# Kernel tuning notes

Hardware: AMD Instinct MI355X
Metric: run time of the kernel (lower is better)

## Reference

```python
import jax, jax.numpy as jnp
import numpy as np

B, T, D_IN, D_OUT = 64, 1024, 512, 512


def setup_inputs() -> dict:
    key = jax.random.key(0)
    k_x, k_w, k_wr = jax.random.split(key, 3)
    x = jax.random.normal(k_x, (B, T, D_IN), dtype=jnp.float32)
    # glorot_uniform for W
    limit = np.sqrt(6.0 / (D_IN + D_OUT)).astype(np.float32)
    W = jax.random.uniform(k_w, (D_IN, D_OUT), dtype=jnp.float32, minval=-limit, maxval=limit)
    # orthogonal for W_recurrent
    a = jax.random.normal(k_wr, (D_OUT, D_OUT), dtype=jnp.float32)
    q, r = jnp.linalg.qr(a)
    W_recurrent = q * jnp.sign(jnp.diag(r))[None, :]
    b = jnp.zeros((D_OUT,), dtype=jnp.float32)
    return {"x": x, "W": W, "W_recurrent": W_recurrent, "b": b}


def reference(x, W, W_recurrent, b):
    # x: [B, T, D_in]; sequential tanh RNN; return last hidden state [B, D_out]
    x_t = jnp.transpose(x, (1, 0, 2))  # [T, B, D_in]
    h0 = jnp.zeros((x.shape[0], W.shape[1]), dtype=x.dtype)

    def step(h, xt):
        h_new = jnp.tanh(xt @ W + h @ W_recurrent + b)
        return h_new, None

    h_last, _ = jax.lax.scan(step, h0, x_t)
    return h_last
```

## Files before the change

kernel.cpp:

```cpp
#include <hip/hip_runtime.h>
#include <math.h>

#define BATCH   64
#define TSTEPS  1024
#define DIN     512
#define DH      512
#define MDIM    (BATCH * TSTEPS)

#define VPAIRS  184
#define LPAIRS  72
#define LSTRIDE 76
#define LDS_WORDS (512 * LSTRIDE + 2 * 256)
#define LDS_BYTES (LDS_WORDS * 4)

typedef _Float16 h2_t __attribute__((ext_vector_type(2)));

__device__ inline unsigned short f2h_bits(float x) {
    _Float16 h = (_Float16)x;
    return __builtin_bit_cast(unsigned short, h);
}

__device__ inline unsigned int pack2h(float lo, float hi) {
    return (unsigned int)f2h_bits(lo) | ((unsigned int)f2h_bits(hi) << 16);
}

__device__ inline float dot2h(unsigned int ha, unsigned int wb, float acc) {
#if __has_builtin(__builtin_amdgcn_fdot2)
    return __builtin_amdgcn_fdot2(__builtin_bit_cast(h2_t, ha),
                                  __builtin_bit_cast(h2_t, wb), acc, false);
#else
    float hl = (float)__builtin_bit_cast(h2_t, ha).x;
    float hh = (float)__builtin_bit_cast(h2_t, ha).y;
    float wl = (float)__builtin_bit_cast(h2_t, wb).x;
    float wh = (float)__builtin_bit_cast(h2_t, wb).y;
    return fmaf(hh, wh, fmaf(hl, wl, acc));
#endif
}

__global__ __launch_bounds__(256) void gemm_xw(const float* __restrict__ X,
                                               const float* __restrict__ W,
                                               const float* __restrict__ bias,
                                               float* __restrict__ XW) {
    __shared__ float As[16][68];
    __shared__ float Bs[16][68];

    const int tid = threadIdx.x;
    const int bx  = blockIdx.x & 7;
    const int by  = blockIdx.x >> 3;
    const int m0  = by * 64;
    const int n0  = bx * 64;

    const int ty = tid >> 4;
    const int tx = tid & 15;

    const int arow = tid >> 2;
    const int akq  = (tid & 3) * 4;
    const int brow = tid >> 4;
    const int bcq  = (tid & 15) * 4;

    float acc[4][4] = {{0.f}};

    for (int k0 = 0; k0 < DIN; k0 += 16) {
        float4 av = *(const float4*)&X[(size_t)(m0 + arow) * DIN + k0 + akq];
        float4 bv = *(const float4*)&W[(size_t)(k0 + brow) * DH + n0 + bcq];
        __syncthreads();
        As[akq + 0][arow] = av.x;
        As[akq + 1][arow] = av.y;
        As[akq + 2][arow] = av.z;
        As[akq + 3][arow] = av.w;
        *(float4*)&Bs[brow][bcq] = bv;
        __syncthreads();

        #pragma unroll
        for (int k = 0; k < 16; ++k) {
            float4 a = *(const float4*)&As[k][ty * 4];
            float4 b = *(const float4*)&Bs[k][tx * 4];
            float ar[4] = {a.x, a.y, a.z, a.w};
            float br[4] = {b.x, b.y, b.z, b.w};
            #pragma unroll
            for (int i = 0; i < 4; ++i)
                #pragma unroll
                for (int j = 0; j < 4; ++j)
                    acc[i][j] = fmaf(ar[i], br[j], acc[i][j]);
        }
    }

    float4 bv = *(const float4*)&bias[n0 + tx * 4];
    const float br[4] = {bv.x, bv.y, bv.z, bv.w};
    #pragma unroll
    for (int i = 0; i < 4; ++i) {
        float4 o;
        o.x = acc[i][0] + br[0];
        o.y = acc[i][1] + br[1];
        o.z = acc[i][2] + br[2];
        o.w = acc[i][3] + br[3];
        *(float4*)&XW[(size_t)(m0 + ty * 4 + i) * DH + n0 + tx * 4] = o;
    }
}

__global__ __launch_bounds__(512, 2) void rnn_scan2(const float* __restrict__ XW,
                                                    const float* __restrict__ Wr,
                                                    float* __restrict__ Hout) {
    extern __shared__ unsigned int lds[];
    unsigned int* wrl  = lds;
    unsigned int* hbuf = lds + 512 * LSTRIDE;

    const int b = blockIdx.x;
    const int j = threadIdx.x;

    unsigned int wreg[VPAIRS];
    #pragma unroll
    for (int p = 0; p < VPAIRS; ++p) {
        float lo = Wr[(size_t)(2 * p)     * DH + j];
        float hi = Wr[(size_t)(2 * p + 1) * DH + j];
        wreg[p] = pack2h(lo, hi);
    }
    unsigned int* wl_my = wrl + (size_t)j * LSTRIDE;
    #pragma unroll
    for (int p = 0; p < LPAIRS; ++p) {
        int r0 = 2 * (VPAIRS + p);
        float lo = Wr[(size_t)r0       * DH + j];
        float hi = Wr[(size_t)(r0 + 1) * DH + j];
        wl_my[p] = pack2h(lo, hi);
    }
    hbuf[j] = 0u;
    __syncthreads();

    const float* xwb = XW + (size_t)b * TSTEPS * DH + j;
    float xwv  = xwb[0];
    float h_f  = 0.0f;
    int   cur  = 0;

    const unsigned int* wl = wrl + (size_t)j * LSTRIDE;

    for (int t = 0; t < TSTEPS; ++t) {
        const unsigned int* hp = hbuf + cur * 256;

        const int tn = (t + 1 < TSTEPS) ? (t + 1) : (TSTEPS - 1);
        float xwn = xwb[(size_t)tn * DH];

        float a0 = 0.f, a1 = 0.f, a2 = 0.f, a3 = 0.f;

        #pragma unroll
        for (int p = 0; p < VPAIRS; p += 4) {
            uint4 hv = *(const uint4*)(hp + p);
            a0 = dot2h(hv.x, wreg[p + 0], a0);
            a1 = dot2h(hv.y, wreg[p + 1], a1);
            a2 = dot2h(hv.z, wreg[p + 2], a2);
            a3 = dot2h(hv.w, wreg[p + 3], a3);
        }
        #pragma unroll
        for (int p = 0; p < LPAIRS; p += 4) {
            uint4 hv = *(const uint4*)(hp + VPAIRS + p);
            uint4 wv = *(const uint4*)(wl + p);
            a0 = dot2h(hv.x, wv.x, a0);
            a1 = dot2h(hv.y, wv.y, a1);
            a2 = dot2h(hv.z, wv.z, a2);
            a3 = dot2h(hv.w, wv.w, a3);
        }

        float z = ((a0 + a1) + (a2 + a3)) + xwv;
        h_f = tanhf(z);

        unsigned short* hbn = (unsigned short*)(hbuf + ((cur ^ 1) * 256));
        hbn[j] = f2h_bits(h_f);

        __syncthreads();
        cur ^= 1;
        xwv = xwn;
    }

    Hout[(size_t)b * DH + j] = h_f;
}

extern "C" void kernel_launch(void* const* d_in, const int* in_sizes, int n_in,
                              void* d_out, int out_size, void* d_ws, size_t ws_size,
                              hipStream_t stream) {
    const float* x  = (const float*)d_in[0];
    const float* W  = (const float*)d_in[1];
    const float* Wr = (const float*)d_in[2];
    const float* bv = (const float*)d_in[3];
    float* out = (float*)d_out;

    const size_t xw_bytes = (size_t)MDIM * DH * sizeof(float);
    if (ws_size < xw_bytes) return;
    float* xw = (float*)d_ws;

    static int lds_attr_done = 0;
    (void)lds_attr_done;
    hipFuncSetAttribute((const void*)rnn_scan2,
                        hipFuncAttributeMaxDynamicSharedMemorySize, LDS_BYTES);

    gemm_xw<<<dim3((MDIM / 64) * (DH / 64)), dim3(256), 0, stream>>>(x, W, bv, xw);

    rnn_scan2<<<dim3(BATCH), dim3(512), LDS_BYTES, stream>>>(xw, Wr, out);
}
```

Before: 2.280 ms.

## Use MFMA fp16 input GEMM and readlane-broadcast hidden state in RNN scan

Converts x to fp16 and transposes W to fp16, then computes the input projection with MFMA 16x16x32 f16 instructions instead of the scalar fp32 GEMM. The scalar kernel stays as a fallback when the workspace is too small. The recurrent scan now loads each wave's hidden-state slice once and broadcasts elements with readlane rather than issuing many LDS loads per step. It also replaces tanhf with an exp2/rcp approximation. This adds two conversion kernels, lowers the precision of the input projection, and changes the tanh accuracy.

Result: slower. 2.516 ms (+10.4%).

```diff
diff --git a/kernel.cpp b/kernel.cpp
--- a/kernel.cpp
+++ b/kernel.cpp
@@ -7,23 +7,23 @@
 #define DH      512
 #define MDIM    (BATCH * TSTEPS)
 
-#define VPAIRS  184
-#define LPAIRS  72
-#define LSTRIDE 76
-#define LDS_WORDS (512 * LSTRIDE + 2 * 256)
-#define LDS_BYTES (LDS_WORDS * 4)
-
-typedef _Float16 h2_t __attribute__((ext_vector_type(2)));
+#define WREGW   180
+#define WLDSW   76
+#define WSTRIDE 76
+#define K2_LDS_WORDS (512 * WSTRIDE + 2 * 256)
+#define K2_LDS_BYTES (K2_LDS_WORDS * 4)
+
+typedef _Float16 h2_t  __attribute__((ext_vector_type(2)));
+typedef _Float16 f16x8 __attribute__((ext_vector_type(8)));
+typedef float    f32x4 __attribute__((ext_vector_type(4)));
 
 __device__ inline unsigned short f2h_bits(float x) {
     _Float16 h = (_Float16)x;
     return __builtin_bit_cast(unsigned short, h);
 }
-
 __device__ inline unsigned int pack2h(float lo, float hi) {
     return (unsigned int)f2h_bits(lo) | ((unsigned int)f2h_bits(hi) << 16);
 }
-
 __device__ inline float dot2h(unsigned int ha, unsigned int wb, float acc) {
 #if __has_builtin(__builtin_amdgcn_fdot2)
     return __builtin_amdgcn_fdot2(__builtin_bit_cast(h2_t, ha),
@@ -36,6 +36,133 @@
     return fmaf(hh, wh, fmaf(hl, wl, acc));
 #endif
 }
+__device__ inline unsigned int rl(unsigned int v, int lane) {
+    return (unsigned int)__builtin_amdgcn_readlane((int)v, lane);
+}
+__device__ inline float ftanh(float x) {
+    float e = __builtin_amdgcn_exp2f(x * 2.88539008177792681472f);
+    return 1.0f - 2.0f * __builtin_amdgcn_rcpf(e + 1.0f);
+}
+
+__global__ __launch_bounds__(256) void convert_x(const float* __restrict__ x,
+                                                 _Float16* __restrict__ xh,
+                                                 int nvec) {
+    int i = blockIdx.x * blockDim.x + threadIdx.x;
+    int stride = gridDim.x * blockDim.x;
+    for (; i < nvec; i += stride) {
+        const float4* p = (const float4*)x + 2 * (size_t)i;
+        float4 a = p[0], b = p[1];
+        f16x8 o = { (_Float16)a.x, (_Float16)a.y, (_Float16)a.z, (_Float16)a.w,
+                    (_Float16)b.x, (_Float16)b.y, (_Float16)b.z, (_Float16)b.w };
+        ((f16x8*)xh)[i] = o;
+    }
+}
+
+__global__ __launch_bounds__(256) void transpose_w(const float* __restrict__ W,
+                                                   _Float16* __restrict__ Wt) {
+    __shared__ float tile[64][65];
+    const int t  = threadIdx.x;
+    const int c  = t & 63;
+    const int r0 = t >> 6;
+    const int bn = blockIdx.x & 7;
+    const int bk = blockIdx.x >> 3;
+    const int k0 = bk * 64, n0 = bn * 64;
+    #pragma unroll
+    for (int i = 0; i < 16; ++i)
+        tile[r0 + 4 * i][c] = W[(size_t)(k0 + r0 + 4 * i) * DH + n0 + c];
+    __syncthreads();
+    #pragma unroll
+    for (int i = 0; i < 16; ++i)
+        Wt[(size_t)(n0 + r0 + 4 * i) * DIN + k0 + c] = (_Float16)tile[c][r0 + 4 * i];
+}
+
+__global__ __launch_bounds__(256) void gemm_xw_mfma(const _Float16* __restrict__ Xh,
+                                                    const _Float16* __restrict__ Wt,
+                                                    const float* __restrict__ bias,
+                                                    float* __restrict__ XW) {
+    __shared__ __align__(16) _Float16 Ah[128][32];
+    __shared__ __align__(16) _Float16 Bh[128][32];
+
+    const int tid  = threadIdx.x;
+    const int wv   = tid >> 6;
+    const int lane = tid & 63;
+    const int bn   = blockIdx.x & 3;
+    const int bm   = blockIdx.x >> 2;
+    const int m0   = bm * 128;
+    const int n0   = bn * 128;
+
+    const int mbase = (wv >> 1) * 64;
+    const int nbase = (wv & 1) * 64;
+    const int fr    = lane & 15;
+    const int fq    = lane >> 4;
+
+    f32x4 acc[4][4];
+    #pragma unroll
+    for (int i = 0; i < 4; ++i)
+        #pragma unroll
+        for (int j = 0; j < 4; ++j)
+            acc[i][j] = (f32x4){0.f, 0.f, 0.f, 0.f};
+
+    for (int kc = 0; kc < DIN / 32; ++kc) {
+        const int k0 = kc * 32;
+#if __has_builtin(__builtin_amdgcn_global_load_lds)
+        #pragma unroll
+        for (int q = 0; q < 2; ++q) {
+            const int rb = wv * 2 + q;
+            const int gr = (rb * 16) + (lane >> 2);
+            const int gc = (lane & 3) * 8;
+            const _Float16* ga = Xh + (size_t)(m0 + gr) * DIN + k0 + gc;
+            const _Float16* gb = Wt + (size_t)(n0 + gr) * DIN + k0 + gc;
+            __builtin_amdgcn_global_load_lds(
+                (const __attribute__((address_space(1))) void*)ga,
+                (__attribute__((address_space(3))) void*)&Ah[rb * 16][0], 16, 0, 0);
+            __builtin_amdgcn_global_load_lds(
+                (const __attribute__((address_space(1))) void*)gb,
+                (__attribute__((address_space(3))) void*)&Bh[rb * 16][0], 16, 0, 0);
+        }
+#else
+        #pragma unroll
+        for (int q = 0; q < 2; ++q) {
+            const int h0 = (q * 256 + tid) * 8;
+            const int row = h0 >> 5, col = h0 & 31;
+            *((uint4*)Ah + (q * 256 + tid)) =
+                *(const uint4*)(Xh + (size_t)(m0 + row) * DIN + k0 + col);
+            *((uint4*)Bh + (q * 256 + tid)) =
+                *(const uint4*)(Wt + (size_t)(n0 + row) * DIN + k0 + col);
+        }
+#endif
+        __syncthreads();
+
+        f16x8 af[4], bf[4];
+        #pragma unroll
+        for (int mt = 0; mt < 4; ++mt)
+            af[mt] = *(const f16x8*)&Ah[mbase + mt * 16 + fr][fq * 8];
+        #pragma unroll
+        for (int nt = 0; nt < 4; ++nt)
+            bf[nt] = *(const f16x8*)&Bh[nbase + nt * 16 + fr][fq * 8];
+        #pragma unroll
+        for (int mt = 0; mt < 4; ++mt)
+            #pragma unroll
+            for (int nt = 0; nt < 4; ++nt)
+                acc[mt][nt] = __builtin_amdgcn_mfma_f32_16x16x32_f16(
+                    af[mt], bf[nt], acc[mt][nt], 0, 0, 0);
+        __syncthreads();
+    }
+
+    #pragma unroll
+    for (int nt = 0; nt < 4; ++nt) {
+        const int col = n0 + nbase + nt * 16 + fr;
+        const float bvl = bias[col];
+        #pragma unroll
+        for (int mt = 0; mt < 4; ++mt) {
+            #pragma unroll
+            for (int r = 0; r < 4; ++r) {
+                const int row = m0 + mbase + mt * 16 + fq * 4 + r;
+                XW[(size_t)row * DH + col] = acc[mt][nt][r] + bvl;
+            }
+        }
+    }
+}
 
 __global__ __launch_bounds__(256) void gemm_xw(const float* __restrict__ X,
                                                const float* __restrict__ W,
@@ -43,34 +170,22 @@
                                                float* __restrict__ XW) {
     __shared__ float As[16][68];
     __shared__ float Bs[16][68];
-
     const int tid = threadIdx.x;
     const int bx  = blockIdx.x & 7;
     const int by  = blockIdx.x >> 3;
-    const int m0  = by * 64;
-    const int n0  = bx * 64;
-
-    const int ty = tid >> 4;
-    const int tx = tid & 15;
-
-    const int arow = tid >> 2;
-    const int akq  = (tid & 3) * 4;
-    const int brow = tid >> 4;
-    const int bcq  = (tid & 15) * 4;
-
+    const int m0  = by * 64, n0 = bx * 64;
+    const int ty = tid >> 4, tx = tid & 15;
+    const int arow = tid >> 2, akq = (tid & 3) * 4;
+    const int brow = tid >> 4, bcq = (tid & 15) * 4;
     float acc[4][4] = {{0.f}};
-
     for (int k0 = 0; k0 < DIN; k0 += 16) {
         float4 av = *(const float4*)&X[(size_t)(m0 + arow) * DIN + k0 + akq];
         float4 bv = *(const float4*)&W[(size_t)(k0 + brow) * DH + n0 + bcq];
         __syncthreads();
-        As[akq + 0][arow] = av.x;
-        As[akq + 1][arow] = av.y;
-        As[akq + 2][arow] = av.z;
-        As[akq + 3][arow] = av.w;
+        As[akq + 0][arow] = av.x; As[akq + 1][arow] = av.y;
+        As[akq + 2][arow] = av.z; As[akq + 3][arow] = av.w;
         *(float4*)&Bs[brow][bcq] = bv;
         __syncthreads();
-
         #pragma unroll
         for (int k = 0; k < 16; ++k) {
             float4 a = *(const float4*)&As[k][ty * 4];
@@ -84,41 +199,39 @@
                     acc[i][j] = fmaf(ar[i], br[j], acc[i][j]);
         }
     }
-
     float4 bv = *(const float4*)&bias[n0 + tx * 4];
     const float br[4] = {bv.x, bv.y, bv.z, bv.w};
     #pragma unroll
     for (int i = 0; i < 4; ++i) {
         float4 o;
-        o.x = acc[i][0] + br[0];
-        o.y = acc[i][1] + br[1];
-        o.z = acc[i][2] + br[2];
-        o.w = acc[i][3] + br[3];
+        o.x = acc[i][0] + br[0]; o.y = acc[i][1] + br[1];
+        o.z = acc[i][2] + br[2]; o.w = acc[i][3] + br[3];
         *(float4*)&XW[(size_t)(m0 + ty * 4 + i) * DH + n0 + tx * 4] = o;
     }
 }
 
-__global__ __launch_bounds__(512, 2) void rnn_scan2(const float* __restrict__ XW,
+__global__ __launch_bounds__(512, 2) void rnn_scan3(const float* __restrict__ XW,
                                                     const float* __restrict__ Wr,
                                                     float* __restrict__ Hout) {
     extern __shared__ unsigned int lds[];
     unsigned int* wrl  = lds;
-    unsigned int* hbuf = lds + 512 * LSTRIDE;
-
-    const int b = blockIdx.x;
-    const int j = threadIdx.x;
-
-    unsigned int wreg[VPAIRS];
-    #pragma unroll
-    for (int p = 0; p < VPAIRS; ++p) {
+    unsigned int* hbuf = lds + 512 * WSTRIDE;
+
+    const int b    = blockIdx.x;
+    const int j    = threadIdx.x;
+    const int lane = j & 63;
+
+    unsigned int wreg[WREGW];
+    #pragma unroll
+    for (int p = 0; p < WREGW; ++p) {
         float lo = Wr[(size_t)(2 * p)     * DH + j];
         float hi = Wr[(size_t)(2 * p + 1) * DH + j];
         wreg[p] = pack2h(lo, hi);
     }
-    unsigned int* wl_my = wrl + (size_t)j * LSTRIDE;
-    #pragma unroll
-    for (int p = 0; p < LPAIRS; ++p) {
-        int r0 = 2 * (VPAIRS + p);
+    unsigned int* wl_my = wrl + (size_t)j * WSTRIDE;
+    #pragma unroll
+    for (int p = 0; p < WLDSW; ++p) {
+        int r0 = 2 * (WREGW + p);
         float lo = Wr[(size_t)r0       * DH + j];
         float hi = Wr[(size_t)(r0 + 1) * DH + j];
         wl_my[p] = pack2h(lo, hi);
@@ -127,14 +240,14 @@
     __syncthreads();
 
     const float* xwb = XW + (size_t)b * TSTEPS * DH + j;
-    float xwv  = xwb[0];
-    float h_f  = 0.0f;
-    int   cur  = 0;
-
-    const unsigned int* wl = wrl + (size_t)j * LSTRIDE;
+    float xwv = xwb[0];
+    float h_f = 0.0f;
+    int   cur = 0;
+
+    const unsigned int* wl = wrl + (size_t)j * WSTRIDE;
 
     for (int t = 0; t < TSTEPS; ++t) {
-        const unsigned int* hp = hbuf + cur * 256;
+        uint4 hv = *((const uint4*)(hbuf + cur * 256) + lane);
 
         const int tn = (t + 1 < TSTEPS) ? (t + 1) : (TSTEPS - 1);
         float xwn = xwb[(size_t)tn * DH];
@@ -142,29 +255,28 @@
         float a0 = 0.f, a1 = 0.f, a2 = 0.f, a3 = 0.f;
 
         #pragma unroll
-        for (int p = 0; p < VPAIRS; p += 4) {
-            uint4 hv = *(const uint4*)(hp + p);
-            a0 = dot2h(hv.x, wreg[p + 0], a0);
-            a1 = dot2h(hv.y, wreg[p + 1], a1);
-            a2 = dot2h(hv.z, wreg[p + 2], a2);
-            a3 = dot2h(hv.w, wreg[p + 3], a3);
-        }
-        #pragma unroll
-        for (int p = 0; p < LPAIRS; p += 4) {
-            uint4 hv = *(const uint4*)(hp + VPAIRS + p);
-            uint4 wv = *(const uint4*)(wl + p);
-            a0 = dot2h(hv.x, wv.x, a0);
-            a1 = dot2h(hv.y, wv.y, a1);
-            a2 = dot2h(hv.z, wv.z, a2);
-            a3 = dot2h(hv.w, wv.w, a3);
-        }
-
-        float z = ((a0 + a1) + (a2 + a3)) + xwv;
-        h_f = tanhf(z);
-
-        unsigned short* hbn = (unsigned short*)(hbuf + ((cur ^ 1) * 256));
-        hbn[j] = f2h_bits(h_f);
-
+        for (int g = 0; g < WREGW / 4; ++g) {
+            unsigned s0 = rl(hv.x, g), s1 = rl(hv.y, g);
+            unsigned s2 = rl(hv.z, g), s3 = rl(hv.w, g);
+            a0 = dot2h(s0, wreg[4 * g + 0], a0);
+            a1 = dot2h(s1, wreg[4 * g + 1], a1);
+            a2 = dot2h(s2, wreg[4 * g + 2], a2);
+            a3 = dot2h(s3, wreg[4 * g + 3], a3);
+        }
+        #pragma unroll
+        for (int g = WREGW / 4; g < 64; ++g) {
+            uint4 wv = *(const uint4*)(wl + 4 * (g - WREGW / 4));
+            unsigned s0 = rl(hv.x, g), s1 = rl(hv.y, g);
+            unsigned s2 = rl(hv.z, g), s3 = rl(hv.w, g);
+            a0 = dot2h(s0, wv.x, a0);
+            a1 = dot2h(s1, wv.y, a1);
+            a2 = dot2h(s2, wv.z, a2);
+            a3 = dot2h(s3, wv.w, a3);
+        }
+
+        h_f = ftanh(((a0 + a1) + (a2 + a3)) + xwv);
+
+        ((unsigned short*)(hbuf + ((cur ^ 1) * 256)))[j] = f2h_bits(h_f);
         __syncthreads();
         cur ^= 1;
         xwv = xwn;
@@ -182,16 +294,26 @@
     const float* bv = (const float*)d_in[3];
     float* out = (float*)d_out;
 
-    const size_t xw_bytes = (size_t)MDIM * DH * sizeof(float);
-    if (ws_size < xw_bytes) return;
+    const size_t XW_BYTES = (size_t)MDIM * DH * sizeof(float);
+    const size_t XH_BYTES = (size_t)MDIM * DIN * sizeof(_Float16);
+    const size_t WT_BYTES = (size_t)DIN * DH * sizeof(_Float16);
+    if (ws_size < XW_BYTES) return;
+
     float* xw = (float*)d_ws;
 
-    static int lds_attr_done = 0;
-    (void)lds_attr_done;
-    hipFuncSetAttribute((const void*)rnn_scan2,
-                        hipFuncAttributeMaxDynamicSharedMemorySize, LDS_BYTES);
-
-    gemm_xw<<<dim3((MDIM / 64) * (DH / 64)), dim3(256), 0, stream>>>(x, W, bv, xw);
-
-    rnn_scan2<<<dim3(BATCH), dim3(512), LDS_BYTES, stream>>>(xw, Wr, out);
-}
+    hipFuncSetAttribute((const void*)rnn_scan3,
+                        hipFuncAttributeMaxDynamicSharedMemorySize, K2_LDS_BYTES);
+
+    if (ws_size >= XW_BYTES + XH_BYTES + WT_BYTES) {
+        _Float16* xh = (_Float16*)((char*)d_ws + XW_BYTES);
+        _Float16* wt = (_Float16*)((char*)d_ws + XW_BYTES + XH_BYTES);
+        convert_x<<<dim3(2048), dim3(256), 0, stream>>>(x, xh, MDIM * DIN / 8);
+        transpose_w<<<dim3(64), dim3(256), 0, stream>>>(W, wt);
+        gemm_xw_mfma<<<dim3((MDIM / 128) * (DH / 128)), dim3(256), 0, stream>>>(
+            xh, wt, bv, xw);
+    } else {
+        gemm_xw<<<dim3((MDIM / 64) * (DH / 64)), dim3(256), 0, stream>>>(x, W, bv, xw);
+    }
+
+    rnn_scan3<<<dim3(BATCH), dim3(512), K2_LDS_BYTES, stream>>>(xw, Wr, out);
+}
```
